# Performance work log

Hardware: AMD Instinct MI355X
Metric: run time of the kernel (lower is better)

The kernel has to match this reference:

```python
import jax, jax.numpy as jnp
import numpy as np

P = 4096      # particles per event
F = 128       # max features per particle (inner ragged axis)
H = 128       # hidden_size


def setup_inputs() -> dict:
    key = jax.random.key(0)
    ks = jax.random.split(key, 12)
    s = 1.0 / np.sqrt(H)  # torch RNN default init scale
    u = lambda k, shp: jax.random.uniform(k, shp, jnp.float32, -s, s)
    event = jax.random.normal(ks[0], (P, F, 1), jnp.float32)
    lengths = jnp.maximum(1, jax.random.randint(ks[1], (P,), 0, F))  # ragged lengths in [1, F)
    return {
        "event": event,
        "lengths": lengths,
        "W_ih1": u(ks[2], (H, 1)), "W_hh1": u(ks[3], (H, H)),
        "b_ih1": u(ks[4], (H,)),   "b_hh1": u(ks[5], (H,)),
        "W_ih2": u(ks[6], (H, H)), "W_hh2": u(ks[7], (H, H)),
        "b_ih2": u(ks[8], (H,)),   "b_hh2": u(ks[9], (H,)),
    }


def reference(event, lengths, W_ih1, W_hh1, b_ih1, b_hh1,
              W_ih2, W_hh2, b_ih2, b_hh2):
    # net1: vanilla tanh RNN over each particle's feature sequence (batched over P).
    # Ragged lengths handled by masking the hidden-state update past each length.
    Pn, Fn, _ = event.shape
    mask = jnp.arange(Fn)[:, None] < lengths[None, :]      # [F, P]
    xs = jnp.transpose(event, (1, 0, 2))                   # [F, P, 1] time-major

    def step1(h, xm):
        x, m = xm                                          # x:[P,1], m:[P]
        h_new = jnp.tanh(x @ W_ih1.T + b_ih1 + h @ W_hh1.T + b_hh1)
        return jnp.where(m[:, None], h_new, h), None

    h0 = jnp.zeros((Pn, H), event.dtype)
    h1, _ = jax.lax.scan(step1, h0, (xs, mask))            # final hidden per particle: [P, H]

    # net2: tanh RNN over the sequence of particle hidden states (unbatched).
    def step2(h, x):
        return jnp.tanh(x @ W_ih2.T + b_ih2 + h @ W_hh2.T + b_hh2), None

    h2, _ = jax.lax.scan(step2, jnp.zeros((H,), event.dtype), h1)
    return h2[None, :]                                     # torch hidden shape (1, H)
```

## Files before the change

kernel.cpp:

```cpp
#include <hip/hip_runtime.h>


constexpr int PN = 4096;
constexpr int FN = 128;
constexpr int HN = 128;
constexpr int CH  = 64;
constexpr int NCH = PN / CH;

__device__ __forceinline__ float fast_tanh(float x) {
    float e = __expf(2.0f * x);
    return 1.0f - 2.0f / (e + 1.0f);
}

__device__ __forceinline__ void lds_barrier() {
    asm volatile("s_waitcnt lgkmcnt(0)\n\ts_barrier" ::: "memory");
}

__device__ __forceinline__ float dpp_xor1(float x) {
    return __int_as_float(__builtin_amdgcn_update_dpp(
        0, __float_as_int(x), 0xB1, 0xF, 0xF, true));
}
__device__ __forceinline__ float dpp_xor2(float x) {
    return __int_as_float(__builtin_amdgcn_update_dpp(
        0, __float_as_int(x), 0x4E, 0xF, 0xF, true));
}
__device__ __forceinline__ float dpp_xor4(float x, bool hi) {
    int a = __builtin_amdgcn_update_dpp(0, __float_as_int(x), 0x104, 0xF, 0xF, true);
    int b = __builtin_amdgcn_update_dpp(0, __float_as_int(x), 0x114, 0xF, 0xF, true);
    return __int_as_float(hi ? b : a);
}
__device__ __forceinline__ float dpp_xor8(float x, bool hi) {
    int a = __builtin_amdgcn_update_dpp(0, __float_as_int(x), 0x108, 0xF, 0xF, true);
    int b = __builtin_amdgcn_update_dpp(0, __float_as_int(x), 0x118, 0xF, 0xF, true);
    return __int_as_float(hi ? b : a);
}

__device__ __forceinline__ float reduce16(const float s[8], int jg) {
    const bool hi8 = (jg & 8) != 0;
    float m0 = hi8 ? s[0] : s[4], k0 = hi8 ? s[4] : s[0];
    float m1 = hi8 ? s[1] : s[5], k1 = hi8 ? s[5] : s[1];
    float m2 = hi8 ? s[2] : s[6], k2 = hi8 ? s[6] : s[2];
    float m3 = hi8 ? s[3] : s[7], k3 = hi8 ? s[7] : s[3];
    float x0 = k0 + dpp_xor8(m0, hi8);
    float x1 = k1 + dpp_xor8(m1, hi8);
    float x2 = k2 + dpp_xor8(m2, hi8);
    float x3 = k3 + dpp_xor8(m3, hi8);
    const bool hi4 = (jg & 4) != 0;
    float y0 = (hi4 ? x2 : x0) + dpp_xor4(hi4 ? x0 : x2, hi4);
    float y1 = (hi4 ? x3 : x1) + dpp_xor4(hi4 ? x1 : x3, hi4);
    const bool hi2 = (jg & 2) != 0;
    float z  = (hi2 ? y1 : y0) + dpp_xor2(hi2 ? y0 : y1);
    z += dpp_xor1(z);
    return z;
}
__device__ __forceinline__ int reduce16_cidx(int jg) {
    return ((jg >> 3) & 1) * 4 + ((jg >> 2) & 1) * 2 + ((jg >> 1) & 1);
}

__device__ __forceinline__ void wait_chunk(const unsigned* cnt, int c) {
    while (__hip_atomic_load(&cnt[c], __ATOMIC_ACQUIRE,
                             __HIP_MEMORY_SCOPE_AGENT) < (unsigned)CH) {
        __builtin_amdgcn_s_sleep(8);
    }
}

template <bool SYNC>
__device__ __forceinline__ void net1_body(
    int p, int tid,
    const float* __restrict__ event,  const int* __restrict__ lengths,
    const float* __restrict__ W_ih1,  const float* __restrict__ W_hh1,
    const float* __restrict__ b_ih1,  const float* __restrict__ b_hh1,
    const float* __restrict__ W_ih2,  const float* __restrict__ b_ih2,
    const float* __restrict__ b_hh2,  float* __restrict__ U,
    unsigned* cnt, float (*h)[HN], float* ev)
{
    const int wv   = tid >> 6;
    const int lane = tid & 63;
    const int jg   = lane & 15;
    const int og16 = (wv << 2) + (lane >> 4);
    const int rot  = (jg >> 2) & 1;
    const int oi_w = og16 * 8 + reduce16_cidx(jg);

    if (tid < FN) ev[tid]   = event[p * FN + tid];
    if (tid < HN) h[0][tid] = 0.0f;

    float w[8][8];
    #pragma unroll
    for (int c = 0; c < 8; ++c) {
        const float* row = W_hh1 + (og16 * 8 + c) * HN + jg * 8;
        #pragma unroll
        for (int t = 0; t < 2; ++t) {
            const int krot = (t + rot) & 1;
            float4 v = *reinterpret_cast<const float4*>(row + 4 * krot);
            w[c][4*t+0] = v.x; w[c][4*t+1] = v.y;
            w[c][4*t+2] = v.z; w[c][4*t+3] = v.w;
        }
    }
    const float wx_own   = W_ih1[oi_w];
    const float bias_own = b_ih1[oi_w] + b_hh1[oi_w];
    const int   len      = lengths[p];

    __syncthreads();

    for (int t = 0; t < len; ++t) {
        const int cur = t & 1;
        const float x = ev[t];
        const float* base = &h[cur][jg * 8];
        float s[8] = {0,0,0,0,0,0,0,0};
        #pragma unroll
        for (int tt = 0; tt < 2; ++tt) {
            const int krot = (tt + rot) & 1;
            float4 hv = *reinterpret_cast<const float4*>(base + 4 * krot);
            #pragma unroll
            for (int c = 0; c < 8; ++c) {
                s[c] = fmaf(w[c][4*tt+0], hv.x, s[c]);
                s[c] = fmaf(w[c][4*tt+1], hv.y, s[c]);
                s[c] = fmaf(w[c][4*tt+2], hv.z, s[c]);
                s[c] = fmaf(w[c][4*tt+3], hv.w, s[c]);
            }
        }
        const float z  = reduce16(s, jg);
        const float hn = fast_tanh(z + fmaf(wx_own, x, bias_own));
        if ((jg & 1) == 0) h[cur ^ 1][oi_w] = hn;
        lds_barrier();
    }

    if (tid < HN) {
        const float4* h4 = reinterpret_cast<const float4*>(h[len & 1]);
        const float4* w2 = reinterpret_cast<const float4*>(W_ih2 + tid * HN);
        float a0 = b_ih2[tid] + b_hh2[tid], a1 = 0.f, a2 = 0.f, a3 = 0.f;
        #pragma unroll
        for (int k = 0; k < HN / 4; ++k) {
            float4 hv = h4[k];
            float4 wv = w2[k];
            a0 = fmaf(wv.x, hv.x, a0);
            a1 = fmaf(wv.y, hv.y, a1);
            a2 = fmaf(wv.z, hv.z, a2);
            a3 = fmaf(wv.w, hv.w, a3);
        }
        U[p * HN + tid] = (a0 + a1) + (a2 + a3);
    }

    if (SYNC) {
        __syncthreads();
        if (tid == 0) {
            __hip_atomic_fetch_add(&cnt[p >> 6], 1u,
                                   __ATOMIC_RELEASE, __HIP_MEMORY_SCOPE_AGENT);
        }
    }
}

template <bool SYNC>
__device__ __forceinline__ void net2_body(
    int tid,
    const float* __restrict__ U, const float* __restrict__ W_hh2,
    float* __restrict__ out, const unsigned* cnt,
    float (*h)[HN], float* Ulds)
{
    const int wv   = tid >> 6;
    const int lane = tid & 63;
    const int jg   = lane & 7;
    const int ogl  = lane >> 3;
    const int og   = (wv << 3) + ogl;
    const int rot  = jg >> 1;
    const bool hi4 = (jg & 4) != 0;
    const int cidx = ((jg >> 2) & 1) * 2 + ((jg >> 1) & 1);
    const int oi_w = og * 4 + cidx;

    __builtin_amdgcn_s_setprio(1);

    float w[4][16];
    #pragma unroll
    for (int c = 0; c < 4; ++c) {
        const float* row = W_hh2 + (og * 4 + c) * HN + jg * 16;
        #pragma unroll
        for (int t = 0; t < 4; ++t) {
            const int krot = (t + rot) & 3;
            float4 v = *reinterpret_cast<const float4*>(row + 4 * krot);
            w[c][4*t+0] = v.x; w[c][4*t+1] = v.y;
            w[c][4*t+2] = v.z; w[c][4*t+3] = v.w;
        }
    }

    if (SYNC) wait_chunk(cnt, 0);
    {
        const float4* g = reinterpret_cast<const float4*>(U);
        float4*       l = reinterpret_cast<float4*>(Ulds);
        #pragma unroll
        for (int r = 0; r < 8; ++r) l[r * 256 + tid] = g[r * 256 + tid];
    }
    if (tid < HN) h[0][tid] = 0.0f;
    __syncthreads();

    for (int c = 0; c < NCH; ++c) {
        const bool has_next = (c + 1 < NCH);
        if (SYNC && has_next) wait_chunk(cnt, c + 1);

        float4 st[8];
        {
            const float4* gsrc = reinterpret_cast<const float4*>(
                U + (has_next ? (c + 1) : c) * CH * HN);
            #pragma unroll
            for (int r = 0; r < 8; ++r) st[r] = gsrc[r * 256 + tid];
        }

        for (int s2 = 0; s2 < CH; ++s2) {
            const int hc = s2 & 1;
            const float u_cur = Ulds[s2 * HN + oi_w];

            const float* base = &h[hc][jg * 16];
            float s0 = 0.f, s1 = 0.f, s2a = 0.f, s3 = 0.f;
            #pragma unroll
            for (int t = 0; t < 4; ++t) {
                const int krot = (t + rot) & 3;
                float4 hv = *reinterpret_cast<const float4*>(base + 4 * krot);
                s0  = fmaf(w[0][4*t+0], hv.x, s0);  s0  = fmaf(w[0][4*t+1], hv.y, s0);
                s0  = fmaf(w[0][4*t+2], hv.z, s0);  s0  = fmaf(w[0][4*t+3], hv.w, s0);
                s1  = fmaf(w[1][4*t+0], hv.x, s1);  s1  = fmaf(w[1][4*t+1], hv.y, s1);
                s1  = fmaf(w[1][4*t+2], hv.z, s1);  s1  = fmaf(w[1][4*t+3], hv.w, s1);
                s2a = fmaf(w[2][4*t+0], hv.x, s2a); s2a = fmaf(w[2][4*t+1], hv.y, s2a);
                s2a = fmaf(w[2][4*t+2], hv.z, s2a); s2a = fmaf(w[2][4*t+3], hv.w, s2a);
                s3  = fmaf(w[3][4*t+0], hv.x, s3);  s3  = fmaf(w[3][4*t+1], hv.y, s3);
                s3  = fmaf(w[3][4*t+2], hv.z, s3);  s3  = fmaf(w[3][4*t+3], hv.w, s3);
            }

            const bool lo4 = !hi4;
            float t0 = lo4 ? s2a : s0;
            float t1 = lo4 ? s3  : s1;
            float x0 = (lo4 ? s0 : s2a) + dpp_xor4(t0, hi4);
            float x1 = (lo4 ? s1 : s3 ) + dpp_xor4(t1, hi4);
            const bool lo2 = (jg & 2) == 0;
            float t2 = lo2 ? x1 : x0;
            float z  = (lo2 ? x0 : x1) + dpp_xor2(t2);
            z += dpp_xor1(z);

            const float hn = fast_tanh(z + u_cur);
            if ((jg & 1) == 0) h[hc ^ 1][oi_w] = hn;
            lds_barrier();
        }
        if (has_next) {
            float4* ldst = reinterpret_cast<float4*>(Ulds);
            #pragma unroll
            for (int r = 0; r < 8; ++r) ldst[r * 256 + tid] = st[r];
        }
        lds_barrier();
    }

    if (tid < HN) out[tid] = h[0][tid];
}

__global__ __launch_bounds__(256) void fused_kernel(
    const float* __restrict__ event,  const int* __restrict__ lengths,
    const float* __restrict__ W_ih1,  const float* __restrict__ W_hh1,
    const float* __restrict__ b_ih1,  const float* __restrict__ b_hh1,
    const float* __restrict__ W_ih2,  const float* __restrict__ W_hh2,
    const float* __restrict__ b_ih2,  const float* __restrict__ b_hh2,
    float* __restrict__ U, float* __restrict__ out, unsigned* cnt)
{
    __shared__ float h[2][HN];
    __shared__ float ev[FN];
    __shared__ float Ulds[CH * HN];

    const int tid = threadIdx.x;
    if (blockIdx.x == 0) {
        net2_body<true>(tid, U, W_hh2, out, cnt, h, Ulds);
    } else {
        net1_body<true>(blockIdx.x - 1, tid, event, lengths, W_ih1, W_hh1,
                        b_ih1, b_hh1, W_ih2, b_ih2, b_hh2, U, cnt, h, ev);
    }
}

__global__ __launch_bounds__(256) void net1_only(
    const float* __restrict__ event,  const int* __restrict__ lengths,
    const float* __restrict__ W_ih1,  const float* __restrict__ W_hh1,
    const float* __restrict__ b_ih1,  const float* __restrict__ b_hh1,
    const float* __restrict__ W_ih2,  const float* __restrict__ b_ih2,
    const float* __restrict__ b_hh2,  float* __restrict__ U)
{
    __shared__ float h[2][HN];
    __shared__ float ev[FN];
    net1_body<false>(blockIdx.x, threadIdx.x, event, lengths, W_ih1, W_hh1,
                     b_ih1, b_hh1, W_ih2, b_ih2, b_hh2, U, nullptr, h, ev);
}

__global__ __launch_bounds__(256) void net2_only(
    const float* __restrict__ U, const float* __restrict__ W_hh2,
    float* __restrict__ out)
{
    __shared__ float h[2][HN];
    __shared__ float Ulds[CH * HN];
    net2_body<false>(threadIdx.x, U, W_hh2, out, nullptr, h, Ulds);
}

extern "C" void kernel_launch(void* const* d_in, const int* in_sizes, int n_in,
                              void* d_out, int out_size, void* d_ws, size_t ws_size,
                              hipStream_t stream)
{
    const float* event   = (const float*)d_in[0];
    const int*   lengths = (const int*)  d_in[1];
    const float* W_ih1   = (const float*)d_in[2];
    const float* W_hh1   = (const float*)d_in[3];
    const float* b_ih1   = (const float*)d_in[4];
    const float* b_hh1   = (const float*)d_in[5];
    const float* W_ih2   = (const float*)d_in[6];
    const float* W_hh2   = (const float*)d_in[7];
    const float* b_ih2   = (const float*)d_in[8];
    const float* b_hh2   = (const float*)d_in[9];
    float* out = (float*)d_out;
    float* U   = (float*)d_ws;
    unsigned* cnt = (unsigned*)(U + (size_t)PN * HN);

    const bool sync_ok =
        ws_size >= (size_t)PN * HN * sizeof(float) + NCH * sizeof(unsigned);

    if (sync_ok) {
        hipMemsetAsync(cnt, 0, NCH * sizeof(unsigned), stream);
        fused_kernel<<<dim3(PN + 1), dim3(256), 0, stream>>>(
            event, lengths, W_ih1, W_hh1, b_ih1, b_hh1,
            W_ih2, W_hh2, b_ih2, b_hh2, U, out, cnt);
    } else {
        net1_only<<<dim3(PN), dim3(256), 0, stream>>>(
            event, lengths, W_ih1, W_hh1, b_ih1, b_hh1, W_ih2, b_ih2, b_hh2, U);
        net2_only<<<dim3(1), dim3(256), 0, stream>>>(U, W_hh2, out);
    }
}
```

Baseline: 1.557 ms.

## Shrink blocks to 128 threads with 8x16 weight tiles per thread

Both RNN stages now use 128-thread blocks. Each thread holds an 8-row by 16-column slice of the recurrent weights in registers, and an 8-lane DPP reduction produces one output per thread. This replaces the 16-lane reduction and the half-idle lanes of the 256-thread layout, so each step needs fewer cross-lane shuffles and two waves per barrier instead of four. The cost is twice as many FMAs per thread and much higher register pressure (128 weight floats). Under launch bounds (128,2) that pressure could spill or limit occupancy for the 4096 net1 blocks.

```diff
diff --git a/kernel.cpp b/kernel.cpp
--- a/kernel.cpp
+++ b/kernel.cpp
@@ -29,38 +29,55 @@
     int b = __builtin_amdgcn_update_dpp(0, __float_as_int(x), 0x114, 0xF, 0xF, true);
     return __int_as_float(hi ? b : a);
 }
-__device__ __forceinline__ float dpp_xor8(float x, bool hi) {
-    int a = __builtin_amdgcn_update_dpp(0, __float_as_int(x), 0x108, 0xF, 0xF, true);
-    int b = __builtin_amdgcn_update_dpp(0, __float_as_int(x), 0x118, 0xF, 0xF, true);
-    return __int_as_float(hi ? b : a);
-}
-
-__device__ __forceinline__ float reduce16(const float s[8], int jg) {
-    const bool hi8 = (jg & 8) != 0;
-    float m0 = hi8 ? s[0] : s[4], k0 = hi8 ? s[4] : s[0];
-    float m1 = hi8 ? s[1] : s[5], k1 = hi8 ? s[5] : s[1];
-    float m2 = hi8 ? s[2] : s[6], k2 = hi8 ? s[6] : s[2];
-    float m3 = hi8 ? s[3] : s[7], k3 = hi8 ? s[7] : s[3];
-    float x0 = k0 + dpp_xor8(m0, hi8);
-    float x1 = k1 + dpp_xor8(m1, hi8);
-    float x2 = k2 + dpp_xor8(m2, hi8);
-    float x3 = k3 + dpp_xor8(m3, hi8);
+
+__device__ __forceinline__ float reduce8(const float s[8], int jg) {
     const bool hi4 = (jg & 4) != 0;
-    float y0 = (hi4 ? x2 : x0) + dpp_xor4(hi4 ? x0 : x2, hi4);
-    float y1 = (hi4 ? x3 : x1) + dpp_xor4(hi4 ? x1 : x3, hi4);
+    float x0 = (hi4 ? s[4] : s[0]) + dpp_xor4(hi4 ? s[0] : s[4], hi4);
+    float x1 = (hi4 ? s[5] : s[1]) + dpp_xor4(hi4 ? s[1] : s[5], hi4);
+    float x2 = (hi4 ? s[6] : s[2]) + dpp_xor4(hi4 ? s[2] : s[6], hi4);
+    float x3 = (hi4 ? s[7] : s[3]) + dpp_xor4(hi4 ? s[3] : s[7], hi4);
     const bool hi2 = (jg & 2) != 0;
-    float z  = (hi2 ? y1 : y0) + dpp_xor2(hi2 ? y0 : y1);
-    z += dpp_xor1(z);
-    return z;
-}
-__device__ __forceinline__ int reduce16_cidx(int jg) {
-    return ((jg >> 3) & 1) * 4 + ((jg >> 2) & 1) * 2 + ((jg >> 1) & 1);
+    float y0 = (hi2 ? x2 : x0) + dpp_xor2(hi2 ? x0 : x2);
+    float y1 = (hi2 ? x3 : x1) + dpp_xor2(hi2 ? x1 : x3);
+    const bool hi1 = (jg & 1) != 0;
+    return (hi1 ? y1 : y0) + dpp_xor1(hi1 ? y0 : y1);
 }
 
 __device__ __forceinline__ void wait_chunk(const unsigned* cnt, int c) {
     while (__hip_atomic_load(&cnt[c], __ATOMIC_ACQUIRE,
                              __HIP_MEMORY_SCOPE_AGENT) < (unsigned)CH) {
         __builtin_amdgcn_s_sleep(8);
+    }
+}
+
+__device__ __forceinline__ void load_w(const float* W, int og, int jg, int rot,
+                                       float w[8][16]) {
+    #pragma unroll
+    for (int c = 0; c < 8; ++c) {
+        const float* row = W + (og * 8 + c) * HN + jg * 16;
+        #pragma unroll
+        for (int t = 0; t < 4; ++t) {
+            const int krot = (t + rot) & 3;
+            float4 v = *reinterpret_cast<const float4*>(row + 4 * krot);
+            w[c][4*t+0] = v.x; w[c][4*t+1] = v.y;
+            w[c][4*t+2] = v.z; w[c][4*t+3] = v.w;
+        }
+    }
+}
+
+__device__ __forceinline__ void matvec_slice(const float* base, int rot,
+                                             const float w[8][16], float s[8]) {
+    #pragma unroll
+    for (int t = 0; t < 4; ++t) {
+        const int krot = (t + rot) & 3;
+        float4 hv = *reinterpret_cast<const float4*>(base + 4 * krot);
+        #pragma unroll
+        for (int c = 0; c < 8; ++c) {
+            s[c] = fmaf(w[c][4*t+0], hv.x, s[c]);
+            s[c] = fmaf(w[c][4*t+1], hv.y, s[c]);
+            s[c] = fmaf(w[c][4*t+2], hv.z, s[c]);
+            s[c] = fmaf(w[c][4*t+3], hv.w, s[c]);
+        }
     }
 }
 
@@ -76,26 +93,16 @@
 {
     const int wv   = tid >> 6;
     const int lane = tid & 63;
-    const int jg   = lane & 15;
-    const int og16 = (wv << 2) + (lane >> 4);
-    const int rot  = (jg >> 2) & 1;
-    const int oi_w = og16 * 8 + reduce16_cidx(jg);
-
-    if (tid < FN) ev[tid]   = event[p * FN + tid];
-    if (tid < HN) h[0][tid] = 0.0f;
-
-    float w[8][8];
-    #pragma unroll
-    for (int c = 0; c < 8; ++c) {
-        const float* row = W_hh1 + (og16 * 8 + c) * HN + jg * 8;
-        #pragma unroll
-        for (int t = 0; t < 2; ++t) {
-            const int krot = (t + rot) & 1;
-            float4 v = *reinterpret_cast<const float4*>(row + 4 * krot);
-            w[c][4*t+0] = v.x; w[c][4*t+1] = v.y;
-            w[c][4*t+2] = v.z; w[c][4*t+3] = v.w;
-        }
-    }
+    const int jg   = lane & 7;
+    const int og   = (wv << 3) + (lane >> 3);
+    const int rot  = jg >> 1;
+    const int oi_w = (wv << 6) + lane;
+
+    ev[tid]   = event[p * FN + tid];
+    h[0][tid] = 0.0f;
+
+    float w[8][16];
+    load_w(W_hh1, og, jg, rot, w);
     const float wx_own   = W_ih1[oi_w];
     const float bias_own = b_ih1[oi_w] + b_hh1[oi_w];
     const int   len      = lengths[p];
@@ -105,38 +112,25 @@
     for (int t = 0; t < len; ++t) {
         const int cur = t & 1;
         const float x = ev[t];
-        const float* base = &h[cur][jg * 8];
         float s[8] = {0,0,0,0,0,0,0,0};
-        #pragma unroll
-        for (int tt = 0; tt < 2; ++tt) {
-            const int krot = (tt + rot) & 1;
-            float4 hv = *reinterpret_cast<const float4*>(base + 4 * krot);
-            #pragma unroll
-            for (int c = 0; c < 8; ++c) {
-                s[c] = fmaf(w[c][4*tt+0], hv.x, s[c]);
-                s[c] = fmaf(w[c][4*tt+1], hv.y, s[c]);
-                s[c] = fmaf(w[c][4*tt+2], hv.z, s[c]);
-                s[c] = fmaf(w[c][4*tt+3], hv.w, s[c]);
-            }
-        }
-        const float z  = reduce16(s, jg);
-        const float hn = fast_tanh(z + fmaf(wx_own, x, bias_own));
-        if ((jg & 1) == 0) h[cur ^ 1][oi_w] = hn;
+        matvec_slice(&h[cur][jg * 16], rot, w, s);
+        const float z  = reduce8(s, jg);
+        h[cur ^ 1][oi_w] = fast_tanh(z + fmaf(wx_own, x, bias_own));
         lds_barrier();
     }
 
-    if (tid < HN) {
+    {
         const float4* h4 = reinterpret_cast<const float4*>(h[len & 1]);
         const float4* w2 = reinterpret_cast<const float4*>(W_ih2 + tid * HN);
         float a0 = b_ih2[tid] + b_hh2[tid], a1 = 0.f, a2 = 0.f, a3 = 0.f;
         #pragma unroll
         for (int k = 0; k < HN / 4; ++k) {
             float4 hv = h4[k];
-            float4 wv = w2[k];
-            a0 = fmaf(wv.x, hv.x, a0);
-            a1 = fmaf(wv.y, hv.y, a1);
-            a2 = fmaf(wv.z, hv.z, a2);
-            a3 = fmaf(wv.w, hv.w, a3);
+            float4 wv2 = w2[k];
+            a0 = fmaf(wv2.x, hv.x, a0);
+            a1 = fmaf(wv2.y, hv.y, a1);
+            a2 = fmaf(wv2.z, hv.z, a2);
+            a3 = fmaf(wv2.w, hv.w, a3);
         }
         U[p * HN + tid] = (a0 + a1) + (a2 + a3);
     }
@@ -160,96 +154,59 @@
     const int wv   = tid >> 6;
     const int lane = tid & 63;
     const int jg   = lane & 7;
-    const int ogl  = lane >> 3;
-    const int og   = (wv << 3) + ogl;
+    const int og   = (wv << 3) + (lane >> 3);
     const int rot  = jg >> 1;
-    const bool hi4 = (jg & 4) != 0;
-    const int cidx = ((jg >> 2) & 1) * 2 + ((jg >> 1) & 1);
-    const int oi_w = og * 4 + cidx;
+    const int oi_w = (wv << 6) + lane;
 
     __builtin_amdgcn_s_setprio(1);
 
-    float w[4][16];
-    #pragma unroll
-    for (int c = 0; c < 4; ++c) {
-        const float* row = W_hh2 + (og * 4 + c) * HN + jg * 16;
-        #pragma unroll
-        for (int t = 0; t < 4; ++t) {
-            const int krot = (t + rot) & 3;
-            float4 v = *reinterpret_cast<const float4*>(row + 4 * krot);
-            w[c][4*t+0] = v.x; w[c][4*t+1] = v.y;
-            w[c][4*t+2] = v.z; w[c][4*t+3] = v.w;
-        }
-    }
+    float w[8][16];
+    load_w(W_hh2, og, jg, rot, w);
 
     if (SYNC) wait_chunk(cnt, 0);
     {
         const float4* g = reinterpret_cast<const float4*>(U);
         float4*       l = reinterpret_cast<float4*>(Ulds);
         #pragma unroll
-        for (int r = 0; r < 8; ++r) l[r * 256 + tid] = g[r * 256 + tid];
-    }
-    if (tid < HN) h[0][tid] = 0.0f;
+        for (int r = 0; r < 16; ++r) l[r * 128 + tid] = g[r * 128 + tid];
+    }
+    h[0][tid] = 0.0f;
     __syncthreads();
 
     for (int c = 0; c < NCH; ++c) {
         const bool has_next = (c + 1 < NCH);
         if (SYNC && has_next) wait_chunk(cnt, c + 1);
 
-        float4 st[8];
+        float4 st[16];
         {
             const float4* gsrc = reinterpret_cast<const float4*>(
                 U + (has_next ? (c + 1) : c) * CH * HN);
             #pragma unroll
-            for (int r = 0; r < 8; ++r) st[r] = gsrc[r * 256 + tid];
+            for (int r = 0; r < 16; ++r) st[r] = gsrc[r * 128 + tid];
         }
 
         for (int s2 = 0; s2 < CH; ++s2) {
             const int hc = s2 & 1;
             const float u_cur = Ulds[s2 * HN + oi_w];
-
-            const float* base = &h[hc][jg * 16];
-            float s0 = 0.f, s1 = 0.f, s2a = 0.f, s3 = 0.f;
-            #pragma unroll
-            for (int t = 0; t < 4; ++t) {
-                const int krot = (t + rot) & 3;
-                float4 hv = *reinterpret_cast<const float4*>(base + 4 * krot);
-                s0  = fmaf(w[0][4*t+0], hv.x, s0);  s0  = fmaf(w[0][4*t+1], hv.y, s0);
-                s0  = fmaf(w[0][4*t+2], hv.z, s0);  s0  = fmaf(w[0][4*t+3], hv.w, s0);
-                s1  = fmaf(w[1][4*t+0], hv.x, s1);  s1  = fmaf(w[1][4*t+1], hv.y, s1);
-                s1  = fmaf(w[1][4*t+2], hv.z, s1);  s1  = fmaf(w[1][4*t+3], hv.w, s1);
-                s2a = fmaf(w[2][4*t+0], hv.x, s2a); s2a = fmaf(w[2][4*t+1], hv.y, s2a);
-                s2a = fmaf(w[2][4*t+2], hv.z, s2a); s2a = fmaf(w[2][4*t+3], hv.w, s2a);
-                s3  = fmaf(w[3][4*t+0], hv.x, s3);  s3  = fmaf(w[3][4*t+1], hv.y, s3);
-                s3  = fmaf(w[3][4*t+2], hv.z, s3);  s3  = fmaf(w[3][4*t+3], hv.w, s3);
-            }
-
-            const bool lo4 = !hi4;
-            float t0 = lo4 ? s2a : s0;
-            float t1 = lo4 ? s3  : s1;
-            float x0 = (lo4 ? s0 : s2a) + dpp_xor4(t0, hi4);
-            float x1 = (lo4 ? s1 : s3 ) + dpp_xor4(t1, hi4);
-            const bool lo2 = (jg & 2) == 0;
-            float t2 = lo2 ? x1 : x0;
-            float z  = (lo2 ? x0 : x1) + dpp_xor2(t2);
-            z += dpp_xor1(z);
-
-            const float hn = fast_tanh(z + u_cur);
-            if ((jg & 1) == 0) h[hc ^ 1][oi_w] = hn;
+            float s[8] = {0,0,0,0,0,0,0,0};
+            matvec_slice(&h[hc][jg * 16], rot, w, s);
+            const float z = reduce8(s, jg);
+            h[hc ^ 1][oi_w] = fast_tanh(z + u_cur);
             lds_barrier();
         }
+
         if (has_next) {
             float4* ldst = reinterpret_cast<float4*>(Ulds);
             #pragma unroll
-            for (int r = 0; r < 8; ++r) ldst[r * 256 + tid] = st[r];
+            for (int r = 0; r < 16; ++r) ldst[r * 128 + tid] = st[r];
         }
         lds_barrier();
     }
 
-    if (tid < HN) out[tid] = h[0][tid];
-}
-
-__global__ __launch_bounds__(256) void fused_kernel(
+    out[tid] = h[0][tid];
+}
+
+__global__ __launch_bounds__(128, 2) void fused_kernel(
     const float* __restrict__ event,  const int* __restrict__ lengths,
     const float* __restrict__ W_ih1,  const float* __restrict__ W_hh1,
     const float* __restrict__ b_ih1,  const float* __restrict__ b_hh1,
@@ -270,7 +227,7 @@
     }
 }
 
-__global__ __launch_bounds__(256) void net1_only(
+__global__ __launch_bounds__(128, 2) void net1_only(
     const float* __restrict__ event,  const int* __restrict__ lengths,
     const float* __restrict__ W_ih1,  const float* __restrict__ W_hh1,
     const float* __restrict__ b_ih1,  const float* __restrict__ b_hh1,
@@ -283,7 +240,7 @@
                      b_ih1, b_hh1, W_ih2, b_ih2, b_hh2, U, nullptr, h, ev);
 }
 
-__global__ __launch_bounds__(256) void net2_only(
+__global__ __launch_bounds__(128, 2) void net2_only(
     const float* __restrict__ U, const float* __restrict__ W_hh2,
     float* __restrict__ out)
 {
@@ -315,12 +272,12 @@
 
     if (sync_ok) {
         hipMemsetAsync(cnt, 0, NCH * sizeof(unsigned), stream);
-        fused_kernel<<<dim3(PN + 1), dim3(256), 0, stream>>>(
+        fused_kernel<<<dim3(PN + 1), dim3(128), 0, stream>>>(
             event, lengths, W_ih1, W_hh1, b_ih1, b_hh1,
             W_ih2, W_hh2, b_ih2, b_hh2, U, out, cnt);
     } else {
-        net1_only<<<dim3(PN), dim3(256), 0, stream>>>(
+        net1_only<<<dim3(PN), dim3(128), 0, stream>>>(
             event, lengths, W_ih1, W_hh1, b_ih1, b_hh1, W_ih2, b_ih2, b_hh2, U);
-        net2_only<<<dim3(1), dim3(256), 0, stream>>>(U, W_hh2, out);
-    }
-}
+        net2_only<<<dim3(1), dim3(128), 0, stream>>>(U, W_hh2, out);
+    }
+}
```

Measured after the change: 1.973 ms. 26.7% more time.
